# Optimization experiments

Measured on AMD Instinct MI355X. Metric: run time of the kernel, lower is better.

The kernel has to match this reference:

```python
import jax, jax.numpy as jnp
import numpy as np

NUM_CLUSTERS = 16
HIDDEN = 1024
BOTTLENECK = 128
N_TOKENS = 65536


def setup_inputs() -> dict:
    key = jax.random.key(0)
    k_h, k_ids, k_w1, k_b1, k_w2, k_b2 = jax.random.split(key, 6)
    h = jax.random.normal(k_h, (N_TOKENS, HIDDEN), dtype=jnp.float32)
    cluster_ids = jax.random.randint(k_ids, (N_TOKENS,), 0, NUM_CLUSTERS)
    # Stacked per-cluster adapter params (torch Linear: y = x @ W.T + b; we store
    # already-transposed weights so forward is x @ W1[c]).
    s1 = 1.0 / np.sqrt(HIDDEN)
    s2 = 1.0 / np.sqrt(BOTTLENECK)
    W1 = jax.random.uniform(k_w1, (NUM_CLUSTERS, HIDDEN, BOTTLENECK), jnp.float32, -s1, s1)
    b1 = jax.random.uniform(k_b1, (NUM_CLUSTERS, BOTTLENECK), jnp.float32, -s1, s1)
    # Original inits these to zero; use small random values so grads are non-trivial.
    W2 = jax.random.uniform(k_w2, (NUM_CLUSTERS, BOTTLENECK, HIDDEN), jnp.float32, -s2, s2) * 0.02
    b2 = jax.random.uniform(k_b2, (NUM_CLUSTERS, HIDDEN), jnp.float32, -s2, s2) * 0.02
    return {"h": h, "cluster_ids": cluster_ids, "W1": W1, "b1": b1, "W2": W2, "b2": b2}


def reference(h, cluster_ids, W1, b1, W2, b2):
    # h: [N, H]; cluster_ids: [N]; W1: [K, H, B]; b1: [K, B]; W2: [K, B, H]; b2: [K, H]
    # out[n] = h[n] + adapter_{cluster_ids[n]}(h[n])
    K = W1.shape[0]
    out = jnp.zeros_like(h)
    for c in range(K):  # fixed small expert count; select per-token result via where
        mid = jax.nn.gelu(h @ W1[c] + b1[c], approximate=False)  # [N, B]
        y = h + mid @ W2[c] + b2[c]                               # [N, H]
        out = jnp.where((cluster_ids == c)[:, None], y, out)
    return out
```

## Files before the change

### kernel.cpp

```cpp
#include <hip/hip_runtime.h>
#include <hip/hip_bf16.h>
#include <math.h>

#define NUM_CLUSTERS 16
#define HIDDEN 1024
#define BOT 128
#define NTOK 65536

typedef __attribute__((ext_vector_type(8))) short bf16x8;
typedef __attribute__((ext_vector_type(4))) float f32x4;

typedef __attribute__((address_space(3))) unsigned int lds_u32;
typedef const __attribute__((address_space(1))) unsigned int glb_u32;

__device__ __forceinline__ void gload16(const void* g, void* l) {
  __builtin_amdgcn_global_load_lds((glb_u32*)g, (lds_u32*)l, 16, 0, 0);
}

__device__ __forceinline__ unsigned short f2bf(float x) {
  union { float f; unsigned u; } v; v.f = x;
  unsigned r = v.u + 0x7fffu + ((v.u >> 16) & 1u);
  return (unsigned short)(r >> 16);
}

__device__ __forceinline__ bf16x8 pack8(float4 a, float4 b) {
  bf16x8 r;
  r[0] = (short)f2bf(a.x); r[1] = (short)f2bf(a.y);
  r[2] = (short)f2bf(a.z); r[3] = (short)f2bf(a.w);
  r[4] = (short)f2bf(b.x); r[5] = (short)f2bf(b.y);
  r[6] = (short)f2bf(b.z); r[7] = (short)f2bf(b.w);
  return r;
}

#define SWZS(row, sidx) ((sidx) ^ (((row) & 7) << 3))

#define SCB() __builtin_amdgcn_sched_barrier(0)
#define VMW(n)                                          \
  do {                                                  \
    SCB();                                              \
    asm volatile("s_waitcnt vmcnt(" #n ")" ::: "memory"); \
    SCB();                                              \
  } while (0)
#define SBAR()                                  \
  do {                                          \
    SCB();                                      \
    __builtin_amdgcn_s_barrier();               \
    SCB();                                      \
  } while (0)
#define LGKM0() asm volatile("s_waitcnt lgkmcnt(0)" ::: "memory")

__device__ __forceinline__ int xcd_swz(int bid, int nwg) {
  const int nx = 8;
  int q = nwg / nx, r = nwg % nx;
  int xcd = bid % nx, idx = bid / nx;
  int b = (xcd < r) ? xcd * (q + 1) : r * (q + 1) + (xcd - r) * q;
  return b + idx;
}


__global__ void k_zero(int* p) {
  if (threadIdx.x < 64) p[threadIdx.x] = 0;
}

__global__ void k_hist(const int* __restrict__ ids, int* __restrict__ counts) {
  __shared__ int lh[NUM_CLUSTERS];
  if (threadIdx.x < NUM_CLUSTERS) lh[threadIdx.x] = 0;
  __syncthreads();
  int i = blockIdx.x * blockDim.x + threadIdx.x;
  int stride = gridDim.x * blockDim.x;
  for (; i < NTOK; i += stride) atomicAdd(&lh[ids[i]], 1);
  __syncthreads();
  if (threadIdx.x < NUM_CLUSTERS) atomicAdd(&counts[threadIdx.x], lh[threadIdx.x]);
}

__global__ void k_scan(const int* __restrict__ counts, int* __restrict__ offsets,
                       int* __restrict__ cursor) {
  if (threadIdx.x == 0 && blockIdx.x == 0) {
    int s = 0;
    for (int c = 0; c < NUM_CLUSTERS; ++c) {
      offsets[c] = s; cursor[c] = s; s += counts[c];
    }
    offsets[NUM_CLUSTERS] = s;
  }
}

__global__ void k_scatter(const int* __restrict__ ids, int* cursor,
                          int* __restrict__ perm) {
  __shared__ int lh[NUM_CLUSTERS], lbase[NUM_CLUSTERS];
  const int tid = threadIdx.x;
  if (tid < NUM_CLUSTERS) lh[tid] = 0;
  __syncthreads();
  const int i = blockIdx.x * 256 + tid;
  const int cc = ids[i];
  const int r = atomicAdd(&lh[cc], 1);
  __syncthreads();
  if (tid < NUM_CLUSTERS) lbase[tid] = atomicAdd(&cursor[tid], lh[tid]);
  __syncthreads();
  perm[lbase[cc] + r] = i;
}

__global__ void k_w1til(const float* __restrict__ W1, unsigned short* __restrict__ outw) {
  const int id = blockIdx.x * 256 + threadIdx.x;
  const int c  = id >> 14;
  const int ks = (id >> 10) & 15;
  const int q  = id & 1023;
  const int o  = q << 4;
  const int row = o >> 7;
  const int lb  = (o & 127) ^ ((row & 7) << 4);
  const int k0  = ks * 64 + (lb >> 1);
  const float* src = W1 + ((size_t)c * HIDDEN + k0) * BOT + row;
  unsigned short v[8];
  #pragma unroll
  for (int j = 0; j < 8; ++j) v[j] = f2bf(src[(size_t)j * BOT]);
  *(uint4*)((char*)outw + ((size_t)(c * 16 + ks)) * 16384 + o) = *(const uint4*)v;
}

__global__ void k_w2lin(const float* __restrict__ W2, unsigned short* __restrict__ outw) {
  const int id = blockIdx.x * 256 + threadIdx.x;
  const int c   = id >> 14;
  const int rem = id & 16383;
  const int fg  = rem >> 6;
  const int l   = rem & 63;
  const int nc  = fg >> 4, kk = (fg >> 2) & 3, nf = fg & 3;
  const int n   = nc * 64 + nf * 16 + (l & 15);
  const int k0  = kk * 32 + (l >> 4) * 8;
  const float* src = W2 + ((size_t)c * BOT + k0) * HIDDEN + n;
  unsigned short v[8];
  #pragma unroll
  for (int j = 0; j < 8; ++j) v[j] = f2bf(src[(size_t)j * HIDDEN]);
  *(uint4*)(outw + (size_t)id * 8) = *(const uint4*)v;
}

__global__ void k_w2til(const float* __restrict__ W2, unsigned short* __restrict__ outw) {
  const int id = blockIdx.x * 256 + threadIdx.x;
  const int c  = id >> 14;
  const int nc = (id >> 10) & 15;
  const int q  = id & 1023;
  const int o  = q << 4;
  const int row = o >> 8;
  const int lb  = (o & 255) ^ ((row & 7) << 4);
  const int b0  = lb >> 1;
  const int n   = nc * 64 + row;
  const float* src = W2 + ((size_t)c * BOT + b0) * HIDDEN + n;
  unsigned short v[8];
  #pragma unroll
  for (int j = 0; j < 8; ++j) v[j] = f2bf(src[(size_t)j * HIDDEN]);
  *(uint4*)((char*)outw + ((size_t)(c * 16 + nc)) * 16384 + o) = *(const uint4*)v;
}

__device__ __forceinline__ bool locate(const int* offsets, int bid, int TMv,
                                       int& c, int& base, int& nvalid) {
  int t = bid;
  for (c = 0; c < NUM_CLUSTERS; ++c) {
    int cnt = offsets[c + 1] - offsets[c];
    int nt = (cnt + TMv - 1) / TMv;
    if (t < nt) {
      base = offsets[c] + t * TMv;
      nvalid = min(TMv, offsets[c + 1] - base);
      return true;
    }
    t -= nt;
  }
  return false;
}


__global__ __launch_bounds__(512, 6) void k_fuse(
    const float* __restrict__ h, const float* __restrict__ b1g,
    const float* __restrict__ b2g, const unsigned short* __restrict__ W1til,
    const unsigned short* __restrict__ W2lin, const int* __restrict__ offsets,
    const int* __restrict__ perm, float* __restrict__ out) {

  __shared__ __align__(16) unsigned short sA[2][4096];
  __shared__ __align__(16) unsigned short sB[2][8192];
  __shared__ int sTok[64];

  const int tid = threadIdx.x;
  const int l = tid & 63, w = tid >> 6;
  const int lr = l & 15, lg = l >> 4;
  const int wr = w >> 2, wc = w & 3;
  const int row = tid >> 3, o8 = tid & 7;

  const int nwg = NTOK / 64 + NUM_CLUSTERS;
  int c, base, nvalid;
  if (!locate(offsets, xcd_swz(blockIdx.x, nwg), 64, c, base, nvalid)) return;

  if (tid < 64) sTok[tid] = perm[base + min(tid, nvalid - 1)];
  LGKM0();
  SBAR();

  const unsigned short* w1base = W1til + (size_t)c * 16 * 8192;
  const unsigned short* wlin   = W2lin + (size_t)c * 131072;
  const float* hrow = h + (long)sTok[row] * HIDDEN + o8 * 8;

  float4 vaA[2], vaB[2];
  vaA[0] = *(const float4*)(hrow);       vaA[1] = *(const float4*)(hrow + 4);
  SCB();
  gload16(w1base + tid * 8, &sB[0][tid * 8]);
  gload16(w1base + 4096 + tid * 8, &sB[0][4096 + tid * 8]);
  SCB();
  vaB[0] = *(const float4*)(hrow + 64);  vaB[1] = *(const float4*)(hrow + 68);
  SCB();
  *(bf16x8*)&sA[0][SWZS(row, row * 64 + o8 * 8)] = pack8(vaA[0], vaA[1]);
  LGKM0();
  VMW(2);
  SBAR();

  f32x4 acc[2][2];
  #pragma unroll
  for (int i = 0; i < 2; ++i)
    #pragma unroll
    for (int j = 0; j < 2; ++j) { f32x4 z = {0.f, 0.f, 0.f, 0.f}; acc[i][j] = z; }

#define G1_MFMA(CUR)                                                          \
  do {                                                                        \
    _Pragma("unroll")                                                         \
    for (int kk = 0; kk < 2; ++kk) {                                          \
      bf16x8 af[2], bfr[2];                                                   \
      _Pragma("unroll")                                                       \
      for (int mf = 0; mf < 2; ++mf) {                                        \
        const int m = wr * 32 + mf * 16 + lr;                                 \
        af[mf] = *(const bf16x8*)&sA[CUR][SWZS(m, m * 64 + kk * 32 + lg * 8)];\
      }                                                                       \
      _Pragma("unroll")                                                       \
      for (int nf = 0; nf < 2; ++nf) {                                        \
        const int rn = wc * 32 + nf * 16 + lr;                                \
        bfr[nf] = *(const bf16x8*)&sB[CUR][SWZS(rn, rn * 64 + kk * 32 + lg * 8)]; \
      }                                                                       \
      _Pragma("unroll")                                                       \
      for (int mf = 0; mf < 2; ++mf)                                          \
        _Pragma("unroll")                                                     \
        for (int nf = 0; nf < 2; ++nf)                                        \
          acc[mf][nf] = __builtin_amdgcn_mfma_f32_16x16x32_bf16(              \
              af[mf], bfr[nf], acc[mf][nf], 0, 0, 0);                         \
    }                                                                         \
  } while (0)

  #pragma unroll
  for (int t = 0; t < 16; ++t) {
    const int cur = t & 1;
    if (t < 15) {
      const unsigned short* w1s = w1base + (t + 1) * 8192;
      gload16(w1s + tid * 8, &sB[cur ^ 1][tid * 8]);
      gload16(w1s + 4096 + tid * 8, &sB[cur ^ 1][4096 + tid * 8]);
      SCB();
    }
    if (t < 14) {
      if (t & 1) {
        vaB[0] = *(const float4*)(hrow + (t + 2) * 64);
        vaB[1] = *(const float4*)(hrow + (t + 2) * 64 + 4);
      } else {
        vaA[0] = *(const float4*)(hrow + (t + 2) * 64);
        vaA[1] = *(const float4*)(hrow + (t + 2) * 64 + 4);
      }
      SCB();
    }
    G1_MFMA(cur);
    if (t < 15) {
      const float4* src = ((t + 1) & 1) ? vaB : vaA;
      *(bf16x8*)&sA[cur ^ 1][SWZS(row, row * 64 + o8 * 8)] = pack8(src[0], src[1]);
      if (t < 14) { VMW(2); } else { VMW(0); }
      LGKM0();
      SBAR();
    }
  }
#undef G1_MFMA

  unsigned short* sMid = &sA[0][0];
  gload16(wlin + tid * 8, &sB[0][tid * 8]);
  gload16(wlin + 4096 + tid * 8, &sB[0][4096 + tid * 8]);
  SCB();
  SBAR();

  {
    float b1v[2];
    #pragma unroll
    for (int nf = 0; nf < 2; ++nf) b1v[nf] = b1g[c * BOT + wc * 32 + nf * 16 + lr];
    #pragma unroll
    for (int mf = 0; mf < 2; ++mf) {
      #pragma unroll
      for (int nf = 0; nf < 2; ++nf) {
        #pragma unroll
        for (int r = 0; r < 4; ++r) {
          float x = acc[mf][nf][r] + b1v[nf];
          float g = 0.5f * x * (1.0f + erff(x * 0.70710678118654752f));
          const int m = wr * 32 + mf * 16 + lg * 4 + r;
          const int n = wc * 32 + nf * 16 + lr;
          sMid[SWZS(m, m * 128 + n)] = f2bf(g);
        }
      }
    }
  }
  LGKM0();
  VMW(0);
  SBAR();

  const int wrow = (w & 3) * 16;
  const int ch = w >> 2;

  bf16x8 ma[4];
  {
    const int mrow = wrow + lr;
    #pragma unroll
    for (int kk = 0; kk < 4; ++kk)
      ma[kk] = *(const bf16x8*)&sMid[SWZS(mrow, mrow * 128 + kk * 32 + lg * 8)];
  }

  const float* hr[4];
  float* orp[4];
  #pragma unroll
  for (int r = 0; r < 4; ++r) {
    const long tk = (long)sTok[wrow + lg * 4 + r] * HIDDEN;
    hr[r] = h + tk;
    orp[r] = out + tk;
  }
  const float* b2c = b2g + c * HIDDEN;

  for (int nc = 0; nc < 16; ++nc) {
    const int cur = nc & 1;
    const int cb = nc * 64 + ch * 32;
    float hv[2][4], bv[2];
    #pragma unroll
    for (int nf = 0; nf < 2; ++nf)
      #pragma unroll
      for (int r = 0; r < 4; ++r)
        hv[nf][r] = hr[r][cb + nf * 16 + lr];
    #pragma unroll
    for (int nf = 0; nf < 2; ++nf) bv[nf] = b2c[cb + nf * 16 + lr];
    SCB();
    if (nc < 15) {
      const unsigned short* ws2 = wlin + (nc + 1) * 8192;
      gload16(ws2 + tid * 8, &sB[cur ^ 1][tid * 8]);
      gload16(ws2 + 4096 + tid * 8, &sB[cur ^ 1][4096 + tid * 8]);
      SCB();
    }

    f32x4 a2[2];
    { f32x4 z = {0.f, 0.f, 0.f, 0.f}; a2[0] = z; a2[1] = z; }
    #pragma unroll
    for (int kk = 0; kk < 4; ++kk) {
      #pragma unroll
      for (int nf = 0; nf < 2; ++nf) {
        const bf16x8 bf =
            *(const bf16x8*)&sB[cur][(kk * 4 + ch * 2 + nf) * 512 + l * 8];
        a2[nf] = __builtin_amdgcn_mfma_f32_16x16x32_bf16(ma[kk], bf, a2[nf], 0, 0, 0);
      }
    }

    #pragma unroll
    for (int nf = 0; nf < 2; ++nf) {
      #pragma unroll
      for (int r = 0; r < 4; ++r) {
        orp[r][cb + nf * 16 + lr] = a2[nf][r] + hv[nf][r] + bv[nf];
      }
    }
    if (nc < 15) {
      VMW(8);
      SBAR();
    }
  }
}

#define FSWZ(row, sidx) ((sidx) ^ (((row) & 7) << 3))

__global__ __launch_bounds__(256, 2) void k_fused(
    const float* __restrict__ h, const float* __restrict__ b1g,
    const float* __restrict__ b2g, const unsigned short* __restrict__ W1til,
    const unsigned short* __restrict__ W2til, const int* __restrict__ offsets,
    const int* __restrict__ perm, float* __restrict__ out) {

  __shared__ __align__(16) unsigned short sAB[16384];
  __shared__ __align__(16) unsigned short sMid[16384];
  __shared__ int sTok[128];

  const int tid = threadIdx.x;
  const int l = tid & 63, w = tid >> 6;
  const int wr = w >> 1, wc = w & 1;
  const int lr = l & 15, lg = l >> 4;

  int c, base, nvalid;
  if (!locate(offsets, blockIdx.x, 128, c, base, nvalid)) return;

  if (tid < 128) sTok[tid] = perm[base + min(tid, nvalid - 1)];
  __syncthreads();

  const unsigned short* w1base = W1til + (size_t)c * 16 * 8192;
  const unsigned short* w2base = W2til + (size_t)c * 16 * 8192;

  const int arow = tid >> 1, ahalf = tid & 1;
  const long htok = (long)sTok[arow] * HIDDEN;

  f32x4 acc[4][4];
  #pragma unroll
  for (int i = 0; i < 4; ++i)
    #pragma unroll
    for (int j = 0; j < 4; ++j) { f32x4 z = {0.f, 0.f, 0.f, 0.f}; acc[i][j] = z; }

  for (int ks = 0; ks < 16; ++ks) {
    __syncthreads();
    const unsigned short* w1s = w1base + ks * 8192;
    #pragma unroll
    for (int j = 0; j < 4; ++j)
      gload16(w1s + j * 2048 + tid * 8, &sAB[8192 + j * 2048 + tid * 8]);
    {
      const float* hp = h + htok + ks * 64 + ahalf * 32;
      float4 v0 = *(const float4*)(hp + 0),  v1 = *(const float4*)(hp + 4);
      float4 v2 = *(const float4*)(hp + 8),  v3 = *(const float4*)(hp + 12);
      float4 v4 = *(const float4*)(hp + 16), v5 = *(const float4*)(hp + 20);
      float4 v6 = *(const float4*)(hp + 24), v7 = *(const float4*)(hp + 28);
      const int sb = arow * 64 + ahalf * 32;
      *(bf16x8*)&sAB[FSWZ(arow, sb + 0)]  = pack8(v0, v1);
      *(bf16x8*)&sAB[FSWZ(arow, sb + 8)]  = pack8(v2, v3);
      *(bf16x8*)&sAB[FSWZ(arow, sb + 16)] = pack8(v4, v5);
      *(bf16x8*)&sAB[FSWZ(arow, sb + 24)] = pack8(v6, v7);
    }
    __syncthreads();
    #pragma unroll
    for (int kk = 0; kk < 2; ++kk) {
      bf16x8 af[4], bfr[4];
      #pragma unroll
      for (int mf = 0; mf < 4; ++mf) {
        const int rw = wr * 64 + mf * 16 + lr;
        af[mf] = *(const bf16x8*)&sAB[FSWZ(rw, rw * 64 + kk * 32 + lg * 8)];
      }
      #pragma unroll
      for (int nf = 0; nf < 4; ++nf) {
        const int rn = wc * 64 + nf * 16 + lr;
        bfr[nf] = *(const bf16x8*)&sAB[8192 + FSWZ(rn, rn * 64 + kk * 32 + lg * 8)];
      }
      #pragma unroll
      for (int mf = 0; mf < 4; ++mf)
        #pragma unroll
        for (int nf = 0; nf < 4; ++nf)
          acc[mf][nf] = __builtin_amdgcn_mfma_f32_16x16x32_bf16(af[mf], bfr[nf], acc[mf][nf], 0, 0, 0);
    }
  }

  float b1v[4];
  #pragma unroll
  for (int nf = 0; nf < 4; ++nf) b1v[nf] = b1g[c * BOT + wc * 64 + nf * 16 + lr];
  #pragma unroll
  for (int mf = 0; mf < 4; ++mf)
    #pragma unroll
    for (int nf = 0; nf < 4; ++nf)
      #pragma unroll
      for (int r = 0; r < 4; ++r) {
        float x = acc[mf][nf][r] + b1v[nf];
        float g = 0.5f * x * (1.0f + erff(x * 0.70710678118654752f));
        const int m = wr * 64 + mf * 16 + lg * 4 + r;
        const int n = wc * 64 + nf * 16 + lr;
        sMid[FSWZ(m, m * 128 + n)] = f2bf(g);
      }

  for (int nc = 0; nc < 16; ++nc) {
    __syncthreads();
    #pragma unroll
    for (int j = 0; j < 4; ++j)
      gload16(w2base + nc * 8192 + j * 2048 + tid * 8, &sAB[j * 2048 + tid * 8]);
    __syncthreads();

    f32x4 a2[4][2];
    #pragma unroll
    for (int i = 0; i < 4; ++i)
      #pragma unroll
      for (int j = 0; j < 2; ++j) { f32x4 z = {0.f, 0.f, 0.f, 0.f}; a2[i][j] = z; }

    #pragma unroll
    for (int kk = 0; kk < 4; ++kk) {
      bf16x8 af[4], bfr[2];
      #pragma unroll
      for (int mf = 0; mf < 4; ++mf) {
        const int m = wr * 64 + mf * 16 + lr;
        af[mf] = *(const bf16x8*)&sMid[FSWZ(m, m * 128 + kk * 32 + lg * 8)];
      }
      #pragma unroll
      for (int nf = 0; nf < 2; ++nf) {
        const int rn = wc * 32 + nf * 16 + lr;
        bfr[nf] = *(const bf16x8*)&sAB[FSWZ(rn, rn * 128 + kk * 32 + lg * 8)];
      }
      #pragma unroll
      for (int mf = 0; mf < 4; ++mf)
        #pragma unroll
        for (int nf = 0; nf < 2; ++nf)
          a2[mf][nf] = __builtin_amdgcn_mfma_f32_16x16x32_bf16(af[mf], bfr[nf], a2[mf][nf], 0, 0, 0);
    }

    #pragma unroll
    for (int nf = 0; nf < 2; ++nf) {
      const int nn = nc * 64 + wc * 32 + nf * 16 + lr;
      const float b2v = b2g[c * HIDDEN + nn];
      #pragma unroll
      for (int mf = 0; mf < 4; ++mf)
        #pragma unroll
        for (int r = 0; r < 4; ++r) {
          const int m = wr * 64 + mf * 16 + lg * 4 + r;
          if (m < nvalid) {
            const long tk = (long)sTok[m] * HIDDEN;
            out[tk + nn] = h[tk + nn] + a2[mf][nf][r] + b2v;
          }
        }
    }
  }
}

extern "C" void kernel_launch(void* const* d_in, const int* in_sizes, int n_in,
                              void* d_out, int out_size, void* d_ws, size_t ws_size,
                              hipStream_t stream) {
  const float* h   = (const float*)d_in[0];
  const int*   ids = (const int*)d_in[1];
  const float* W1  = (const float*)d_in[2];
  const float* b1  = (const float*)d_in[3];
  const float* W2  = (const float*)d_in[4];
  const float* b2  = (const float*)d_in[5];
  float* out = (float*)d_out;

  char* ws = (char*)d_ws;
  int* counts  = (int*)ws;
  int* cursor  = (int*)(ws + 64);
  int* offsets = (int*)(ws + 128);
  int* perm    = (int*)(ws + 256);
  unsigned short* W1til = (unsigned short*)(ws + 262400);
  unsigned short* W2buf = W1til + (size_t)16 * 16 * 8192;
  const size_t need = 262400 + 2 * (size_t)16 * 16 * 8192 * 2;

  k_zero<<<1, 64, 0, stream>>>(counts);
  k_hist<<<256, 256, 0, stream>>>(ids, counts);
  k_scan<<<1, 64, 0, stream>>>(counts, offsets, cursor);
  k_scatter<<<NTOK / 256, 256, 0, stream>>>(ids, cursor, perm);
  k_w1til<<<1024, 256, 0, stream>>>(W1, W1til);

  if (ws_size >= need) {
    k_w2lin<<<1024, 256, 0, stream>>>(W2, W2buf);
    const int nwg = NTOK / 64 + NUM_CLUSTERS;
    k_fuse<<<nwg, 512, 0, stream>>>(h, b1, b2, W1til, W2buf, offsets, perm, out);
  } else {
    k_w2til<<<1024, 256, 0, stream>>>(W2, W2buf);
    k_fused<<<NTOK / 128 + NUM_CLUSTERS, 256, 0, stream>>>(
        h, b1, b2, W1til, W2buf, offsets, perm, out);
  }
}
```

Before: 244.3 us.

## Halve k-step and n-chunk tiles to shrink LDS and raise k_fuse occupancy

The fused adapter kernel now stages 32-wide K slices of W1 and 32-column chunks of W2 instead of 64. Its LDS is packed into one 32 KB buffer in which the GELU mid tile aliases the stage-1 buffers. The launch bound rises to 8 workgroups per CU, with weight pre-layout kernels rewritten to match the new tile shapes. The aim is more resident waves to hide global-memory latency. The cost is twice as many barrier-separated iterations with less MFMA work each, and smaller 4-element h loads and stores.

```diff
diff --git a/kernel.cpp b/kernel.cpp
--- a/kernel.cpp
+++ b/kernel.cpp
@@ -8,6 +8,7 @@
 #define NTOK 65536
 
 typedef __attribute__((ext_vector_type(8))) short bf16x8;
+typedef __attribute__((ext_vector_type(4))) short bf16x4;
 typedef __attribute__((ext_vector_type(4))) float f32x4;
 
 typedef __attribute__((address_space(3))) unsigned int lds_u32;
@@ -21,6 +22,13 @@
   union { float f; unsigned u; } v; v.f = x;
   unsigned r = v.u + 0x7fffu + ((v.u >> 16) & 1u);
   return (unsigned short)(r >> 16);
+}
+
+__device__ __forceinline__ bf16x4 pack4(float4 a) {
+  bf16x4 r;
+  r[0] = (short)f2bf(a.x); r[1] = (short)f2bf(a.y);
+  r[2] = (short)f2bf(a.z); r[3] = (short)f2bf(a.w);
+  return r;
 }
 
 __device__ __forceinline__ bf16x8 pack8(float4 a, float4 b) {
@@ -99,6 +107,37 @@
   perm[lbase[cc] + r] = i;
 }
 
+__global__ void k_w1til32(const float* __restrict__ W1, unsigned short* __restrict__ outw) {
+  const int id = blockIdx.x * 256 + threadIdx.x;
+  const int c   = id >> 14;
+  const int rem = id & 16383;
+  const int ks  = rem >> 9;
+  const int n   = (rem >> 2) & 127;
+  const int lg  = rem & 3;
+  const int k0  = ks * 32 + lg * 8;
+  const float* src = W1 + ((size_t)c * HIDDEN + k0) * BOT + n;
+  unsigned short v[8];
+  #pragma unroll
+  for (int j = 0; j < 8; ++j) v[j] = f2bf(src[(size_t)j * BOT]);
+  const int phys = (n * 64 + lg * 16) ^ ((n & 7) << 4);
+  *(uint4*)((char*)outw + ((size_t)(c * 32 + ks)) * 8192 + phys) = *(const uint4*)v;
+}
+
+__global__ void k_w2lin32(const float* __restrict__ W2, unsigned short* __restrict__ outw) {
+  const int id = blockIdx.x * 256 + threadIdx.x;
+  const int c   = id >> 14;
+  const int fg  = (id >> 6) & 255;
+  const int l   = id & 63;
+  const int nc  = fg >> 3, kk = (fg >> 1) & 3, nf = fg & 1;
+  const int n   = nc * 32 + nf * 16 + (l & 15);
+  const int k0  = kk * 32 + (l >> 4) * 8;
+  const float* src = W2 + ((size_t)c * BOT + k0) * HIDDEN + n;
+  unsigned short v[8];
+  #pragma unroll
+  for (int j = 0; j < 8; ++j) v[j] = f2bf(src[(size_t)j * HIDDEN]);
+  *(uint4*)(outw + (size_t)id * 8) = *(const uint4*)v;
+}
+
 __global__ void k_w1til(const float* __restrict__ W1, unsigned short* __restrict__ outw) {
   const int id = blockIdx.x * 256 + threadIdx.x;
   const int c  = id >> 14;
@@ -113,22 +152,6 @@
   #pragma unroll
   for (int j = 0; j < 8; ++j) v[j] = f2bf(src[(size_t)j * BOT]);
   *(uint4*)((char*)outw + ((size_t)(c * 16 + ks)) * 16384 + o) = *(const uint4*)v;
-}
-
-__global__ void k_w2lin(const float* __restrict__ W2, unsigned short* __restrict__ outw) {
-  const int id = blockIdx.x * 256 + threadIdx.x;
-  const int c   = id >> 14;
-  const int rem = id & 16383;
-  const int fg  = rem >> 6;
-  const int l   = rem & 63;
-  const int nc  = fg >> 4, kk = (fg >> 2) & 3, nf = fg & 3;
-  const int n   = nc * 64 + nf * 16 + (l & 15);
-  const int k0  = kk * 32 + (l >> 4) * 8;
-  const float* src = W2 + ((size_t)c * BOT + k0) * HIDDEN + n;
-  unsigned short v[8];
-  #pragma unroll
-  for (int j = 0; j < 8; ++j) v[j] = f2bf(src[(size_t)j * HIDDEN]);
-  *(uint4*)(outw + (size_t)id * 8) = *(const uint4*)v;
 }
 
 __global__ void k_w2til(const float* __restrict__ W2, unsigned short* __restrict__ outw) {
@@ -165,21 +188,25 @@
 }
 
 
-__global__ __launch_bounds__(512, 6) void k_fuse(
+__global__ __launch_bounds__(512, 8) void k_fuse(
     const float* __restrict__ h, const float* __restrict__ b1g,
     const float* __restrict__ b2g, const unsigned short* __restrict__ W1til,
     const unsigned short* __restrict__ W2lin, const int* __restrict__ offsets,
     const int* __restrict__ perm, float* __restrict__ out) {
 
-  __shared__ __align__(16) unsigned short sA[2][4096];
-  __shared__ __align__(16) unsigned short sB[2][8192];
+  __shared__ __align__(16) unsigned char sLds[32768];
   __shared__ int sTok[64];
+
+#define SA(cur)  ((unsigned short*)(sLds + (cur) * 4096))
+#define SB1(cur) ((unsigned short*)(sLds + 8192 + (cur) * 8192))
+#define SMID     ((unsigned short*)sLds)
+#define SB2(cur) ((unsigned short*)(sLds + 16384 + (cur) * 8192))
 
   const int tid = threadIdx.x;
   const int l = tid & 63, w = tid >> 6;
   const int lr = l & 15, lg = l >> 4;
   const int wr = w >> 2, wc = w & 3;
-  const int row = tid >> 3, o8 = tid & 7;
+  const int row = tid >> 3, o4 = tid & 7;
 
   const int nwg = NTOK / 64 + NUM_CLUSTERS;
   int c, base, nvalid;
@@ -189,21 +216,20 @@
   LGKM0();
   SBAR();
 
-  const unsigned short* w1base = W1til + (size_t)c * 16 * 8192;
+  const unsigned short* w1base = W1til + (size_t)c * 131072;
   const unsigned short* wlin   = W2lin + (size_t)c * 131072;
-  const float* hrow = h + (long)sTok[row] * HIDDEN + o8 * 8;
-
-  float4 vaA[2], vaB[2];
-  vaA[0] = *(const float4*)(hrow);       vaA[1] = *(const float4*)(hrow + 4);
+  const float* hrow = h + (long)sTok[row] * HIDDEN + o4 * 4;
+
+  float4 vaA, vaB;
+  vaA = *(const float4*)(hrow);
   SCB();
-  gload16(w1base + tid * 8, &sB[0][tid * 8]);
-  gload16(w1base + 4096 + tid * 8, &sB[0][4096 + tid * 8]);
+  gload16(w1base + tid * 8, SB1(0) + tid * 8);
   SCB();
-  vaB[0] = *(const float4*)(hrow + 64);  vaB[1] = *(const float4*)(hrow + 68);
+  vaB = *(const float4*)(hrow + 32);
   SCB();
-  *(bf16x8*)&sA[0][SWZS(row, row * 64 + o8 * 8)] = pack8(vaA[0], vaA[1]);
+  *(bf16x4*)&SA(0)[SWZS(row, row * 32 + o4 * 4)] = pack4(vaA);
   LGKM0();
-  VMW(2);
+  VMW(1);
   SBAR();
 
   f32x4 acc[2][2];
@@ -212,65 +238,49 @@
     #pragma unroll
     for (int j = 0; j < 2; ++j) { f32x4 z = {0.f, 0.f, 0.f, 0.f}; acc[i][j] = z; }
 
-#define G1_MFMA(CUR)                                                          \
-  do {                                                                        \
-    _Pragma("unroll")                                                         \
-    for (int kk = 0; kk < 2; ++kk) {                                          \
-      bf16x8 af[2], bfr[2];                                                   \
-      _Pragma("unroll")                                                       \
-      for (int mf = 0; mf < 2; ++mf) {                                        \
-        const int m = wr * 32 + mf * 16 + lr;                                 \
-        af[mf] = *(const bf16x8*)&sA[CUR][SWZS(m, m * 64 + kk * 32 + lg * 8)];\
-      }                                                                       \
-      _Pragma("unroll")                                                       \
-      for (int nf = 0; nf < 2; ++nf) {                                        \
-        const int rn = wc * 32 + nf * 16 + lr;                                \
-        bfr[nf] = *(const bf16x8*)&sB[CUR][SWZS(rn, rn * 64 + kk * 32 + lg * 8)]; \
-      }                                                                       \
-      _Pragma("unroll")                                                       \
-      for (int mf = 0; mf < 2; ++mf)                                          \
-        _Pragma("unroll")                                                     \
-        for (int nf = 0; nf < 2; ++nf)                                        \
-          acc[mf][nf] = __builtin_amdgcn_mfma_f32_16x16x32_bf16(              \
-              af[mf], bfr[nf], acc[mf][nf], 0, 0, 0);                         \
-    }                                                                         \
-  } while (0)
-
-  #pragma unroll
-  for (int t = 0; t < 16; ++t) {
+  #pragma unroll
+  for (int t = 0; t < 32; ++t) {
     const int cur = t & 1;
-    if (t < 15) {
-      const unsigned short* w1s = w1base + (t + 1) * 8192;
-      gload16(w1s + tid * 8, &sB[cur ^ 1][tid * 8]);
-      gload16(w1s + 4096 + tid * 8, &sB[cur ^ 1][4096 + tid * 8]);
+    if (t < 31) {
+      gload16(w1base + (t + 1) * 4096 + tid * 8, SB1(cur ^ 1) + tid * 8);
       SCB();
     }
-    if (t < 14) {
-      if (t & 1) {
-        vaB[0] = *(const float4*)(hrow + (t + 2) * 64);
-        vaB[1] = *(const float4*)(hrow + (t + 2) * 64 + 4);
-      } else {
-        vaA[0] = *(const float4*)(hrow + (t + 2) * 64);
-        vaA[1] = *(const float4*)(hrow + (t + 2) * 64 + 4);
-      }
+    if (t < 30) {
+      if (t & 1) vaB = *(const float4*)(hrow + (t + 2) * 32);
+      else       vaA = *(const float4*)(hrow + (t + 2) * 32);
       SCB();
     }
-    G1_MFMA(cur);
-    if (t < 15) {
-      const float4* src = ((t + 1) & 1) ? vaB : vaA;
-      *(bf16x8*)&sA[cur ^ 1][SWZS(row, row * 64 + o8 * 8)] = pack8(src[0], src[1]);
-      if (t < 14) { VMW(2); } else { VMW(0); }
+    {
+      bf16x8 af[2], bfr[2];
+      #pragma unroll
+      for (int mf = 0; mf < 2; ++mf) {
+        const int m = wr * 32 + mf * 16 + lr;
+        af[mf] = *(const bf16x8*)&SA(cur)[SWZS(m, m * 32 + lg * 8)];
+      }
+      #pragma unroll
+      for (int nf = 0; nf < 2; ++nf) {
+        const int rn = wc * 32 + nf * 16 + lr;
+        bfr[nf] = *(const bf16x8*)&SB1(cur)[SWZS(rn, rn * 32 + lg * 8)];
+      }
+      #pragma unroll
+      for (int mf = 0; mf < 2; ++mf)
+        #pragma unroll
+        for (int nf = 0; nf < 2; ++nf)
+          acc[mf][nf] = __builtin_amdgcn_mfma_f32_16x16x32_bf16(
+              af[mf], bfr[nf], acc[mf][nf], 0, 0, 0);
+    }
+    if (t < 31) {
+      const float4 src = ((t + 1) & 1) ? vaB : vaA;
+      *(bf16x4*)&SA(cur ^ 1)[SWZS(row, row * 32 + o4 * 4)] = pack4(src);
+      if (t < 30) { VMW(1); } else { VMW(0); }
       LGKM0();
       SBAR();
     }
   }
-#undef G1_MFMA
-
-  unsigned short* sMid = &sA[0][0];
-  gload16(wlin + tid * 8, &sB[0][tid * 8]);
-  gload16(wlin + 4096 + tid * 8, &sB[0][4096 + tid * 8]);
+
+  SBAR();
+  gload16(wlin + tid * 8, SB2(0) + tid * 8);
   SCB();
-  SBAR();
 
   {
     float b1v[2];
@@ -286,7 +296,7 @@
           float g = 0.5f * x * (1.0f + erff(x * 0.70710678118654752f));
           const int m = wr * 32 + mf * 16 + lg * 4 + r;
           const int n = wc * 32 + nf * 16 + lr;
-          sMid[SWZS(m, m * 128 + n)] = f2bf(g);
+          SMID[SWZS(m, m * 128 + n)] = f2bf(g);
         }
       }
     }
@@ -303,7 +313,7 @@
     const int mrow = wrow + lr;
     #pragma unroll
     for (int kk = 0; kk < 4; ++kk)
-      ma[kk] = *(const bf16x8*)&sMid[SWZS(mrow, mrow * 128 + kk * 32 + lg * 8)];
+      ma[kk] = *(const bf16x8*)&SMID[SWZS(mrow, mrow * 128 + kk * 32 + lg * 8)];
   }
 
   const float* hr[4];
@@ -316,49 +326,39 @@
   }
   const float* b2c = b2g + c * HIDDEN;
 
-  for (int nc = 0; nc < 16; ++nc) {
+  for (int nc = 0; nc < 32; ++nc) {
     const int cur = nc & 1;
-    const int cb = nc * 64 + ch * 32;
-    float hv[2][4], bv[2];
-    #pragma unroll
-    for (int nf = 0; nf < 2; ++nf)
-      #pragma unroll
-      for (int r = 0; r < 4; ++r)
-        hv[nf][r] = hr[r][cb + nf * 16 + lr];
-    #pragma unroll
-    for (int nf = 0; nf < 2; ++nf) bv[nf] = b2c[cb + nf * 16 + lr];
+    const int cb = nc * 32 + ch * 16;
+    float hv[4], bv;
+    #pragma unroll
+    for (int r = 0; r < 4; ++r) hv[r] = hr[r][cb + lr];
+    bv = b2c[cb + lr];
     SCB();
-    if (nc < 15) {
-      const unsigned short* ws2 = wlin + (nc + 1) * 8192;
-      gload16(ws2 + tid * 8, &sB[cur ^ 1][tid * 8]);
-      gload16(ws2 + 4096 + tid * 8, &sB[cur ^ 1][4096 + tid * 8]);
+    if (nc < 31) {
+      gload16(wlin + (nc + 1) * 4096 + tid * 8, SB2(cur ^ 1) + tid * 8);
       SCB();
     }
 
-    f32x4 a2[2];
-    { f32x4 z = {0.f, 0.f, 0.f, 0.f}; a2[0] = z; a2[1] = z; }
+    f32x4 a2 = {0.f, 0.f, 0.f, 0.f};
     #pragma unroll
     for (int kk = 0; kk < 4; ++kk) {
-      #pragma unroll
-      for (int nf = 0; nf < 2; ++nf) {
-        const bf16x8 bf =
-            *(const bf16x8*)&sB[cur][(kk * 4 + ch * 2 + nf) * 512 + l * 8];
-        a2[nf] = __builtin_amdgcn_mfma_f32_16x16x32_bf16(ma[kk], bf, a2[nf], 0, 0, 0);
-      }
-    }
-
-    #pragma unroll
-    for (int nf = 0; nf < 2; ++nf) {
-      #pragma unroll
-      for (int r = 0; r < 4; ++r) {
-        orp[r][cb + nf * 16 + lr] = a2[nf][r] + hv[nf][r] + bv[nf];
-      }
-    }
-    if (nc < 15) {
-      VMW(8);
+      const bf16x8 bf = *(const bf16x8*)&SB2(cur)[(kk * 2 + ch) * 512 + l * 8];
+      a2 = __builtin_amdgcn_mfma_f32_16x16x32_bf16(ma[kk], bf, a2, 0, 0, 0);
+    }
+
+    #pragma unroll
+    for (int r = 0; r < 4; ++r)
+      orp[r][cb + lr] = a2[r] + hv[r] + bv;
+
+    if (nc < 31) {
+      VMW(4);
       SBAR();
     }
   }
+#undef SA
+#undef SB1
+#undef SMID
+#undef SB2
 }
 
 #define FSWZ(row, sidx) ((sidx) ^ (((row) & 7) << 3))
@@ -519,23 +519,24 @@
   int* cursor  = (int*)(ws + 64);
   int* offsets = (int*)(ws + 128);
   int* perm    = (int*)(ws + 256);
-  unsigned short* W1til = (unsigned short*)(ws + 262400);
-  unsigned short* W2buf = W1til + (size_t)16 * 16 * 8192;
+  unsigned short* W1buf = (unsigned short*)(ws + 262400);
+  unsigned short* W2buf = W1buf + (size_t)16 * 16 * 8192;
   const size_t need = 262400 + 2 * (size_t)16 * 16 * 8192 * 2;
 
   k_zero<<<1, 64, 0, stream>>>(counts);
   k_hist<<<256, 256, 0, stream>>>(ids, counts);
   k_scan<<<1, 64, 0, stream>>>(counts, offsets, cursor);
   k_scatter<<<NTOK / 256, 256, 0, stream>>>(ids, cursor, perm);
-  k_w1til<<<1024, 256, 0, stream>>>(W1, W1til);
 
   if (ws_size >= need) {
-    k_w2lin<<<1024, 256, 0, stream>>>(W2, W2buf);
+    k_w1til32<<<1024, 256, 0, stream>>>(W1, W1buf);
+    k_w2lin32<<<1024, 256, 0, stream>>>(W2, W2buf);
     const int nwg = NTOK / 64 + NUM_CLUSTERS;
-    k_fuse<<<nwg, 512, 0, stream>>>(h, b1, b2, W1til, W2buf, offsets, perm, out);
+    k_fuse<<<nwg, 512, 0, stream>>>(h, b1, b2, W1buf, W2buf, offsets, perm, out);
   } else {
+    k_w1til<<<1024, 256, 0, stream>>>(W1, W1buf);
     k_w2til<<<1024, 256, 0, stream>>>(W2, W2buf);
     k_fused<<<NTOK / 128 + NUM_CLUSTERS, 256, 0, stream>>>(
-        h, b1, b2, W1til, W2buf, offsets, perm, out);
-  }
-}
+        h, b1, b2, W1buf, W2buf, offsets, perm, out);
+  }
+}
```

Measured after the change: 281.9 us. 15.4% more time.

## Replace atomic token bucketing with deterministic per-block count, scan and stable scatter

Applied to the files above, without the earlier changes.

Rewrites the token-to-cluster permutation as a three-kernel pipeline: per-block histograms, a single-block scan producing per-block bases and cluster offsets, and a stable scatter that ranks tokens within each block by counting earlier matches in shared memory. This drops the zero and histogram kernels and the global atomics, going from four preprocessing launches to three and making token order within each cluster deterministic and sorted. The cost is a serial 256-step scan per cluster in one small block and an O(256) rank loop per thread. The scatter order may also change memory locality for the main fused kernel's gathers.

```diff
diff --git a/kernel.cpp b/kernel.cpp
--- a/kernel.cpp
+++ b/kernel.cpp
@@ -58,45 +58,53 @@
 }
 
 
-__global__ void k_zero(int* p) {
-  if (threadIdx.x < 64) p[threadIdx.x] = 0;
-}
-
-__global__ void k_hist(const int* __restrict__ ids, int* __restrict__ counts) {
+__global__ void k_bcnt(const int* __restrict__ ids, int* __restrict__ bcnt) {
   __shared__ int lh[NUM_CLUSTERS];
-  if (threadIdx.x < NUM_CLUSTERS) lh[threadIdx.x] = 0;
-  __syncthreads();
-  int i = blockIdx.x * blockDim.x + threadIdx.x;
-  int stride = gridDim.x * blockDim.x;
-  for (; i < NTOK; i += stride) atomicAdd(&lh[ids[i]], 1);
-  __syncthreads();
-  if (threadIdx.x < NUM_CLUSTERS) atomicAdd(&counts[threadIdx.x], lh[threadIdx.x]);
-}
-
-__global__ void k_scan(const int* __restrict__ counts, int* __restrict__ offsets,
-                       int* __restrict__ cursor) {
-  if (threadIdx.x == 0 && blockIdx.x == 0) {
-    int s = 0;
-    for (int c = 0; c < NUM_CLUSTERS; ++c) {
-      offsets[c] = s; cursor[c] = s; s += counts[c];
-    }
-    offsets[NUM_CLUSTERS] = s;
-  }
-}
-
-__global__ void k_scatter(const int* __restrict__ ids, int* cursor,
-                          int* __restrict__ perm) {
-  __shared__ int lh[NUM_CLUSTERS], lbase[NUM_CLUSTERS];
-  const int tid = threadIdx.x;
+  const int tid = threadIdx.x, b = blockIdx.x;
   if (tid < NUM_CLUSTERS) lh[tid] = 0;
   __syncthreads();
-  const int i = blockIdx.x * 256 + tid;
-  const int cc = ids[i];
-  const int r = atomicAdd(&lh[cc], 1);
+  atomicAdd(&lh[ids[b * 256 + tid]], 1);
   __syncthreads();
-  if (tid < NUM_CLUSTERS) lbase[tid] = atomicAdd(&cursor[tid], lh[tid]);
+  if (tid < NUM_CLUSTERS) bcnt[tid * 256 + b] = lh[tid];
+}
+
+__global__ void k_bscan(const int* __restrict__ bcnt, int* __restrict__ bbase,
+                        int* __restrict__ offsets) {
+  __shared__ int tot[NUM_CLUSTERS];
+  const int tid = threadIdx.x;
+  if (tid < NUM_CLUSTERS) {
+    int s = 0;
+    for (int b = 0; b < 256; ++b) {
+      bbase[tid * 256 + b] = s;
+      s += bcnt[tid * 256 + b];
+    }
+    tot[tid] = s;
+  }
   __syncthreads();
-  perm[lbase[cc] + r] = i;
+  if (tid == 0) {
+    int s = 0;
+    for (int c = 0; c < NUM_CLUSTERS; ++c) { offsets[c] = s; s += tot[c]; }
+    offsets[NUM_CLUSTERS] = s;
+  }
+  __syncthreads();
+  if (tid < NUM_CLUSTERS) {
+    const int base = offsets[tid];
+    for (int b = 0; b < 256; ++b) bbase[tid * 256 + b] += base;
+  }
+}
+
+__global__ void k_sscat(const int* __restrict__ ids, const int* __restrict__ bbase,
+                        int* __restrict__ perm) {
+  __shared__ int sIds[256];
+  const int tid = threadIdx.x, b = blockIdx.x;
+  const int i = b * 256 + tid;
+  const int c = ids[i];
+  sIds[tid] = c;
+  __syncthreads();
+  int rank = 0;
+  #pragma unroll 8
+  for (int j = 0; j < 256; ++j) rank += (j < tid && sIds[j] == c) ? 1 : 0;
+  perm[bbase[c * 256 + b] + rank] = i;
 }
 
 __global__ void k_w1til(const float* __restrict__ W1, unsigned short* __restrict__ outw) {
@@ -163,7 +171,6 @@
   }
   return false;
 }
-
 
 __global__ __launch_bounds__(512, 6) void k_fuse(
     const float* __restrict__ h, const float* __restrict__ b1g,
@@ -515,27 +522,26 @@
   float* out = (float*)d_out;
 
   char* ws = (char*)d_ws;
-  int* counts  = (int*)ws;
-  int* cursor  = (int*)(ws + 64);
   int* offsets = (int*)(ws + 128);
   int* perm    = (int*)(ws + 256);
-  unsigned short* W1til = (unsigned short*)(ws + 262400);
-  unsigned short* W2buf = W1til + (size_t)16 * 16 * 8192;
-  const size_t need = 262400 + 2 * (size_t)16 * 16 * 8192 * 2;
-
-  k_zero<<<1, 64, 0, stream>>>(counts);
-  k_hist<<<256, 256, 0, stream>>>(ids, counts);
-  k_scan<<<1, 64, 0, stream>>>(counts, offsets, cursor);
-  k_scatter<<<NTOK / 256, 256, 0, stream>>>(ids, cursor, perm);
-  k_w1til<<<1024, 256, 0, stream>>>(W1, W1til);
+  int* bcnt    = (int*)(ws + 262400);
+  int* bbase   = (int*)(ws + 262400 + 16384);
+  unsigned short* W1buf = (unsigned short*)(ws + 262400 + 32768);
+  unsigned short* W2buf = W1buf + (size_t)16 * 16 * 8192;
+  const size_t need = 262400 + 32768 + 2 * (size_t)16 * 16 * 8192 * 2;
+
+  k_bcnt<<<256, 256, 0, stream>>>(ids, bcnt);
+  k_bscan<<<1, 64, 0, stream>>>(bcnt, bbase, offsets);
+  k_sscat<<<256, 256, 0, stream>>>(ids, bbase, perm);
+  k_w1til<<<1024, 256, 0, stream>>>(W1, W1buf);
 
   if (ws_size >= need) {
     k_w2lin<<<1024, 256, 0, stream>>>(W2, W2buf);
     const int nwg = NTOK / 64 + NUM_CLUSTERS;
-    k_fuse<<<nwg, 512, 0, stream>>>(h, b1, b2, W1til, W2buf, offsets, perm, out);
+    k_fuse<<<nwg, 512, 0, stream>>>(h, b1, b2, W1buf, W2buf, offsets, perm, out);
   } else {
     k_w2til<<<1024, 256, 0, stream>>>(W2, W2buf);
     k_fused<<<NTOK / 128 + NUM_CLUSTERS, 256, 0, stream>>>(
-        h, b1, b2, W1til, W2buf, offsets, perm, out);
-  }
-}
+        h, b1, b2, W1buf, W2buf, offsets, perm, out);
+  }
+}
```

Measured after the change: 253.5 us. +3.7%, slower.
